# Kernel optimization log

Hardware: AMD Instinct MI355X
Metric: run time of the kernel (lower is better)

The kernel has to match this reference:

```python
import jax, jax.numpy as jnp
import numpy as np

N = 50000
DIM = 512
HID = 256
NCLS = 2
E = 800000


def gcn_conv(x, W, b, src, dst, deg_inv_sqrt, num_nodes):
    # GCNConv (PyG default): h = D^{-1/2} (A + I) D^{-1/2} x W + b
    h = x @ W  # [N, out]
    norm = deg_inv_sqrt[src] * deg_inv_sqrt[dst]  # [E+N]
    msgs = norm[:, None] * h[src]  # gather per edge
    out = jax.ops.segment_sum(msgs, dst, num_segments=num_nodes)
    return out + b


def setup_inputs() -> dict:
    key = jax.random.key(0)
    k1, k2, k3, k4 = jax.random.split(key, 4)
    x = jax.random.normal(k1, (N, DIM), dtype=jnp.float32)
    edge_index = jax.random.randint(k2, (2, E), 0, N, dtype=jnp.int64)
    # Glorot-style init for weights, zero bias (as PyG GCNConv)
    W1 = jax.random.normal(k3, (DIM, HID), dtype=jnp.float32) * (1.0 / np.sqrt(DIM))
    b1 = jnp.zeros((HID,), dtype=jnp.float32)
    W2 = jax.random.normal(k4, (HID, NCLS), dtype=jnp.float32) * (1.0 / np.sqrt(HID))
    b2 = jnp.zeros((NCLS,), dtype=jnp.float32)
    return {"x": x, "W1": W1, "b1": b1, "W2": W2, "b2": b2, "edge_index": edge_index}


def reference(x, W1, b1, W2, b2, edge_index):
    num_nodes = x.shape[0]
    loops = jnp.arange(num_nodes, dtype=edge_index.dtype)
    src = jnp.concatenate([edge_index[0], loops])
    dst = jnp.concatenate([edge_index[1], loops])
    # symmetric normalization with self-loops (edge_weight = 1)
    deg = jax.ops.segment_sum(jnp.ones_like(dst, dtype=x.dtype), dst, num_segments=num_nodes)
    deg_inv_sqrt = jnp.where(deg > 0, jax.lax.rsqrt(deg), 0.0)

    h = gcn_conv(x, W1, b1, src, dst, deg_inv_sqrt, num_nodes)
    h = jax.nn.relu(h)
    # dropout p=0.5 is identity at inference (training=False)
    out = gcn_conv(h, W2, b2, src, dst, deg_inv_sqrt, num_nodes)
    return out
```

## Files before the change

### kernel.cpp

```cpp
#include <hip/hip_runtime.h>
#include <stdint.h>

#define NN   50000
#define DIMK 512
#define HIDN 256
#define NE   800000

#define SCAN_ITEMS 4
#define SCAN_BLK 256
#define SCAN_PER_BLOCK (SCAN_ITEMS * SCAN_BLK)
#define NBLK ((NN + SCAN_PER_BLOCK - 1) / SCAN_PER_BLOCK)

typedef float f32x4  __attribute__((ext_vector_type(4)));
typedef float f32x16 __attribute__((ext_vector_type(16)));
typedef short s16x8  __attribute__((ext_vector_type(8)));

static __device__ __forceinline__ unsigned short f2bf(float f) {
  union { float f; uint32_t u; } v; v.f = f;
  uint32_t u = v.u;
  u += 0x7fffu + ((u >> 16) & 1u);
  return (unsigned short)(u >> 16);
}

static __device__ __forceinline__ uint32_t cvt_pk_bf16(float lo, float hi) {
  uint32_t r;
  asm("v_cvt_pk_bf16_f32 %0, %1, %2" : "=v"(r) : "v"(lo), "v"(hi));
  return r;
}

__global__ void k_hist(const int* __restrict__ edst, int* __restrict__ cnt) {
  int e = blockIdx.x * 256 + threadIdx.x;
  if (e < NE) atomicAdd(&cnt[edst[e]], 1);
}

__global__ __launch_bounds__(256) void k_blocksum(const int* __restrict__ cnt,
                                                  int* __restrict__ blocksum) {
  const int t = threadIdx.x;
  const int base = blockIdx.x * SCAN_PER_BLOCK + t * SCAN_ITEMS;
  int s = 0;
#pragma unroll
  for (int j = 0; j < SCAN_ITEMS; ++j) { int i = base + j; if (i < NN) s += cnt[i]; }
#pragma unroll
  for (int o = 1; o < 64; o <<= 1) s += __shfl_xor(s, o);
  __shared__ int wsum[4];
  if ((t & 63) == 0) wsum[t >> 6] = s;
  __syncthreads();
  if (t == 0) blocksum[blockIdx.x] = wsum[0] + wsum[1] + wsum[2] + wsum[3];
}

__global__ void k_scanblocks(const int* __restrict__ blocksum, int* __restrict__ blockoff) {
  const int t = threadIdx.x;
  int own = (t < NBLK) ? blocksum[t] : 0;
  int v = own;
#pragma unroll
  for (int o = 1; o < 64; o <<= 1) { int u = __shfl_up(v, o); if (t >= o) v += u; }
  if (t < NBLK) blockoff[t] = v - own;
}

__global__ __launch_bounds__(256) void k_finalize(const int* __restrict__ cnt,
                                                  const int* __restrict__ blockoff,
                                                  int* __restrict__ offsets,
                                                  int* __restrict__ cursor,
                                                  float* __restrict__ dis) {
  const int t = threadIdx.x;
  const int l = t & 63, w = t >> 6;
  const int base = blockIdx.x * SCAN_PER_BLOCK + t * SCAN_ITEMS;
  int c[SCAN_ITEMS]; int s = 0;
#pragma unroll
  for (int j = 0; j < SCAN_ITEMS; ++j) { int i = base + j; c[j] = (i < NN) ? cnt[i] : 0; s += c[j]; }
  const int own = s;
#pragma unroll
  for (int o = 1; o < 64; o <<= 1) { int u = __shfl_up(s, o); if (l >= o) s += u; }
  __shared__ int wt[4];
  if (l == 63) wt[w] = s;
  __syncthreads();
  int waveoff = 0;
  for (int ww = 0; ww < w; ++ww) waveoff += wt[ww];
  int run = blockoff[blockIdx.x] + waveoff + (s - own);
#pragma unroll
  for (int j = 0; j < SCAN_ITEMS; ++j) {
    int i = base + j;
    if (i < NN) {
      offsets[i] = run;
      cursor[i]  = run;
      dis[i] = rsqrtf((float)(c[j] + 1));
      run += c[j];
    }
  }
  if (blockIdx.x == 0 && t == 0) offsets[NN] = NE;
}

__global__ void k_scatter(const int* __restrict__ esrc, const int* __restrict__ edst,
                          int* __restrict__ cursor, int* __restrict__ ssorted) {
  int e = blockIdx.x * 256 + threadIdx.x;
  if (e < NE) {
    int d = edst[e];
    int p = atomicAdd(&cursor[d], 1);
    ssorted[p] = esrc[e];
  }
}

__global__ void k_prep_w1t(const float* __restrict__ W1, char* __restrict__ w1t) {
  int tid = blockIdx.x * 256 + threadIdx.x;
  int c  = tid & 255;
  int k  = tid >> 8;
  int t  = k >> 4;
  int kk = k & 15;
  int g  = kk >> 3;
  int i  = kk & 7;
  int j  = c >> 5;
  int cc = c & 31;
  unsigned short v = f2bf(W1[k * HIDN + c]);
  *(unsigned short*)(w1t + (t * 8 + j) * 1024 + (g * 32 + cc) * 16 + i * 2) = v;
}

#define GSTEP(T, AC, BC)                                                        \
  {                                                                             \
    union { s16x8 v; uint32_t u[4]; } AF;                                       \
    AF.u[0] = cvt_pk_bf16(AC[0].x, AC[0].y);                                    \
    AF.u[1] = cvt_pk_bf16(AC[0].z, AC[0].w);                                    \
    AF.u[2] = cvt_pk_bf16(AC[1].x, AC[1].y);                                    \
    AF.u[3] = cvt_pk_bf16(AC[1].z, AC[1].w);                                    \
    _Pragma("unroll")                                                           \
    for (int j = 0; j < 4; ++j)                                                 \
      acc[j] = __builtin_amdgcn_mfma_f32_32x32x16_bf16(AF.v, BC[j], acc[j], 0, 0, 0); \
    if ((T) + 2 < 32) {                                                         \
      _Pragma("unroll")                                                         \
      for (int j = 0; j < 4; ++j)                                               \
        BC[j] = *(const s16x8*)(wb + ((T) + 2) * 8192 + j * 1024);              \
    }                                                                           \
    if ((T) + 4 < 32) {                                                         \
      AC[0] = ap[((T) + 4) * 4];                                                \
      AC[1] = ap[((T) + 4) * 4 + 1];                                            \
    }                                                                           \
  }

__global__ __launch_bounds__(256, 3) void k_gemm1(const float* __restrict__ x,
                                                  const char* __restrict__ w1t,
                                                  const float* __restrict__ dis,
                                                  unsigned short* __restrict__ h1s) {
  const int l = threadIdx.x & 63;
  const int wid = (blockIdx.x * 256 + threadIdx.x) >> 6;
  const int stripe = wid >> 1;
  const int R0 = stripe * 32;
  if (R0 >= NN) return;
  const int j0 = (wid & 1) * 4;
  const int h = l >> 5;
  int ra = R0 + (l & 31);
  if (ra >= NN) ra = NN - 1;

  const float4* ap = (const float4*)(x + (size_t)ra * DIMK) + h * 2;
  const char* wb = w1t + j0 * 1024 + l * 16;

  f32x16 acc[4];
#pragma unroll
  for (int j = 0; j < 4; ++j)
#pragma unroll
    for (int g = 0; g < 16; ++g) acc[j][g] = 0.f;

  float4 A0[2], A1[2], A2[2], A3[2];
  A0[0] = ap[0];  A0[1] = ap[1];
  A1[0] = ap[4];  A1[1] = ap[5];
  A2[0] = ap[8];  A2[1] = ap[9];
  A3[0] = ap[12]; A3[1] = ap[13];
  s16x8 Ba[4], Bb[4];
#pragma unroll
  for (int j = 0; j < 4; ++j) Ba[j] = *(const s16x8*)(wb + j * 1024);
#pragma unroll
  for (int j = 0; j < 4; ++j) Bb[j] = *(const s16x8*)(wb + 8192 + j * 1024);

#pragma unroll
  for (int q = 0; q < 8; ++q) {
    GSTEP(4 * q + 0, A0, Ba);
    GSTEP(4 * q + 1, A1, Bb);
    GSTEP(4 * q + 2, A2, Ba);
    GSTEP(4 * q + 3, A3, Bb);
  }

  const int cc = l & 31;
  float dv[16];
#pragma unroll
  for (int g = 0; g < 16; ++g) {
    int row = R0 + (g & 3) + 8 * (g >> 2) + 4 * h;
    dv[g] = (row < NN) ? dis[row] : 0.f;
  }
#pragma unroll
  for (int j = 0; j < 4; ++j) {
#pragma unroll
    for (int g = 0; g < 16; ++g) {
      int row = R0 + (g & 3) + 8 * (g >> 2) + 4 * h;
      if (row < NN)
        h1s[(size_t)row * HIDN + (j0 + j) * 32 + cc] = f2bf(acc[j][g] * dv[g]);
    }
  }
}

__global__ __launch_bounds__(256) void k_agg1(const unsigned short* __restrict__ h1s,
                                              const int* __restrict__ offsets,
                                              const int* __restrict__ ssorted,
                                              const float* __restrict__ dis,
                                              const float* __restrict__ b1,
                                              const float* __restrict__ W2,
                                              float* __restrict__ h2s) {
  const int w = threadIdx.x >> 6;
  const int l = threadIdx.x & 63;
  const int d = blockIdx.x * 4 + w;
  if (d >= NN) return;

  float a0, a1, a2, a3;
  {
    uint2 v = *(const uint2*)(h1s + (size_t)d * HIDN + l * 4);
    a0 = __uint_as_float(v.x << 16);
    a1 = __uint_as_float(v.x & 0xffff0000u);
    a2 = __uint_as_float(v.y << 16);
    a3 = __uint_as_float(v.y & 0xffff0000u);
  }
  const int off0 = offsets[d], off1 = offsets[d + 1];
  int e = off0;
  for (; e + 4 <= off1; e += 4) {
    int s0 = ssorted[e], s1 = ssorted[e + 1], s2 = ssorted[e + 2], s3 = ssorted[e + 3];
    uint2 v0 = *(const uint2*)(h1s + (size_t)s0 * HIDN + l * 4);
    uint2 v1 = *(const uint2*)(h1s + (size_t)s1 * HIDN + l * 4);
    uint2 v2 = *(const uint2*)(h1s + (size_t)s2 * HIDN + l * 4);
    uint2 v3 = *(const uint2*)(h1s + (size_t)s3 * HIDN + l * 4);
    a0 += __uint_as_float(v0.x << 16) + __uint_as_float(v1.x << 16) +
          __uint_as_float(v2.x << 16) + __uint_as_float(v3.x << 16);
    a1 += __uint_as_float(v0.x & 0xffff0000u) + __uint_as_float(v1.x & 0xffff0000u) +
          __uint_as_float(v2.x & 0xffff0000u) + __uint_as_float(v3.x & 0xffff0000u);
    a2 += __uint_as_float(v0.y << 16) + __uint_as_float(v1.y << 16) +
          __uint_as_float(v2.y << 16) + __uint_as_float(v3.y << 16);
    a3 += __uint_as_float(v0.y & 0xffff0000u) + __uint_as_float(v1.y & 0xffff0000u) +
          __uint_as_float(v2.y & 0xffff0000u) + __uint_as_float(v3.y & 0xffff0000u);
  }
  for (; e < off1; ++e) {
    int s = ssorted[e];
    uint2 v = *(const uint2*)(h1s + (size_t)s * HIDN + l * 4);
    a0 += __uint_as_float(v.x << 16);
    a1 += __uint_as_float(v.x & 0xffff0000u);
    a2 += __uint_as_float(v.y << 16);
    a3 += __uint_as_float(v.y & 0xffff0000u);
  }

  const float dsd = dis[d];
  const int c0 = l * 4;
  float r0 = fmaxf(a0 * dsd + b1[c0 + 0], 0.f);
  float r1 = fmaxf(a1 * dsd + b1[c0 + 1], 0.f);
  float r2 = fmaxf(a2 * dsd + b1[c0 + 2], 0.f);
  float r3 = fmaxf(a3 * dsd + b1[c0 + 3], 0.f);

  float p0 = r0 * W2[(c0 + 0) * 2] + r1 * W2[(c0 + 1) * 2] +
             r2 * W2[(c0 + 2) * 2] + r3 * W2[(c0 + 3) * 2];
  float p1 = r0 * W2[(c0 + 0) * 2 + 1] + r1 * W2[(c0 + 1) * 2 + 1] +
             r2 * W2[(c0 + 2) * 2 + 1] + r3 * W2[(c0 + 3) * 2 + 1];
#pragma unroll
  for (int o = 1; o < 64; o <<= 1) {
    p0 += __shfl_xor(p0, o);
    p1 += __shfl_xor(p1, o);
  }
  if (l == 0) {
    h2s[(size_t)d * 2 + 0] = dsd * p0;
    h2s[(size_t)d * 2 + 1] = dsd * p1;
  }
}

__global__ void k_agg2(const float* __restrict__ h2s, const int* __restrict__ offsets,
                       const int* __restrict__ ssorted, const float* __restrict__ dis,
                       const float* __restrict__ b2, float* __restrict__ out) {
  int d = blockIdx.x * 256 + threadIdx.x;
  if (d >= NN) return;
  float2 sv = *(const float2*)(h2s + (size_t)d * 2);
  float a0 = sv.x, a1 = sv.y;
  int off0 = offsets[d], off1 = offsets[d + 1];
  int e = off0;
  for (; e + 4 <= off1; e += 4) {
    int s0 = ssorted[e], s1 = ssorted[e + 1], s2 = ssorted[e + 2], s3 = ssorted[e + 3];
    float2 v0 = *(const float2*)(h2s + (size_t)s0 * 2);
    float2 v1 = *(const float2*)(h2s + (size_t)s1 * 2);
    float2 v2 = *(const float2*)(h2s + (size_t)s2 * 2);
    float2 v3 = *(const float2*)(h2s + (size_t)s3 * 2);
    a0 += v0.x + v1.x + v2.x + v3.x;
    a1 += v0.y + v1.y + v2.y + v3.y;
  }
  for (; e < off1; ++e) {
    int s = ssorted[e];
    float2 v = *(const float2*)(h2s + (size_t)s * 2);
    a0 += v.x; a1 += v.y;
  }
  float dsd = dis[d];
  out[(size_t)d * 2 + 0] = dsd * a0 + b2[0];
  out[(size_t)d * 2 + 1] = dsd * a1 + b2[1];
}

extern "C" void kernel_launch(void* const* d_in, const int* in_sizes, int n_in,
                              void* d_out, int out_size, void* d_ws, size_t ws_size,
                              hipStream_t stream) {
  (void)in_sizes; (void)n_in; (void)out_size; (void)ws_size;
  const float* x   = (const float*)d_in[0];
  const float* W1  = (const float*)d_in[1];
  const float* b1  = (const float*)d_in[2];
  const float* W2  = (const float*)d_in[3];
  const float* b2  = (const float*)d_in[4];
  const int*   ei  = (const int*)d_in[5];
  const int* esrc = ei;
  const int* edst = ei + NE;
  float* out = (float*)d_out;

  char* ws = (char*)d_ws;
  unsigned short* h1s = (unsigned short*)(ws + 0);
  char*  w1t     = ws + 25600000;
  float* dis     = (float*)(ws + 25862144);
  float* h2s     = (float*)(ws + 26062144);
  int*   cnt     = (int*)(ws + 26462144);
  int*   offsets = (int*)(ws + 26662144);
  int*   cursor  = (int*)(ws + 26862208);
  int*   ssorted = (int*)(ws + 27062208);
  int*   blocksum= (int*)(ws + 30262208);
  int*   blockoff= (int*)(ws + 30262464);

  hipMemsetAsync(cnt, 0, NN * sizeof(int), stream);
  k_hist<<<(NE + 255) / 256, 256, 0, stream>>>(edst, cnt);
  k_blocksum<<<NBLK, 256, 0, stream>>>(cnt, blocksum);
  k_scanblocks<<<1, 64, 0, stream>>>(blocksum, blockoff);
  k_finalize<<<NBLK, 256, 0, stream>>>(cnt, blockoff, offsets, cursor, dis);
  k_scatter<<<(NE + 255) / 256, 256, 0, stream>>>(esrc, edst, cursor, ssorted);
  k_prep_w1t<<<(DIMK * HIDN) / 256, 256, 0, stream>>>(W1, w1t);
  {
    const int nwaves = 2 * ((NN + 31) / 32);
    const int nblk   = (nwaves + 3) / 4;
    k_gemm1<<<nblk, 256, 0, stream>>>(x, w1t, dis, h1s);
  }
  k_agg1<<<(NN + 3) / 4, 256, 0, stream>>>(h1s, offsets, ssorted, dis, b1, W2, h2s);
  k_agg2<<<(NN + 255) / 256, 256, 0, stream>>>(h2s, offsets, ssorted, dis, b2, out);
}
```

Before: 214.8 us.

## Stage x tiles through LDS with coalesced loads in GEMM1, one wave per block

GEMM1 now launches one 64-thread wave per block. It loads x rows cooperatively with coalesced float4 reads into a padded LDS tile (stride 17), prefetching the next K-tile into registers, then reads the MFMA A fragments from LDS. Before, each lane read two float4s directly from its own row, which gave strided uncoalesced accesses. The change adds two barriers per K-tile and LDS traffic, and 64-thread blocks may limit occupancy packing. Both waves of a stripe still load the same x rows independently.

```diff
diff --git a/kernel.cpp b/kernel.cpp
--- a/kernel.cpp
+++ b/kernel.cpp
@@ -114,42 +114,31 @@
   *(unsigned short*)(w1t + (t * 8 + j) * 1024 + (g * 32 + cc) * 16 + i * 2) = v;
 }
 
-#define GSTEP(T, AC, BC)                                                        \
-  {                                                                             \
-    union { s16x8 v; uint32_t u[4]; } AF;                                       \
-    AF.u[0] = cvt_pk_bf16(AC[0].x, AC[0].y);                                    \
-    AF.u[1] = cvt_pk_bf16(AC[0].z, AC[0].w);                                    \
-    AF.u[2] = cvt_pk_bf16(AC[1].x, AC[1].y);                                    \
-    AF.u[3] = cvt_pk_bf16(AC[1].z, AC[1].w);                                    \
-    _Pragma("unroll")                                                           \
-    for (int j = 0; j < 4; ++j)                                                 \
-      acc[j] = __builtin_amdgcn_mfma_f32_32x32x16_bf16(AF.v, BC[j], acc[j], 0, 0, 0); \
-    if ((T) + 2 < 32) {                                                         \
-      _Pragma("unroll")                                                         \
-      for (int j = 0; j < 4; ++j)                                               \
-        BC[j] = *(const s16x8*)(wb + ((T) + 2) * 8192 + j * 1024);              \
-    }                                                                           \
-    if ((T) + 4 < 32) {                                                         \
-      AC[0] = ap[((T) + 4) * 4];                                                \
-      AC[1] = ap[((T) + 4) * 4 + 1];                                            \
-    }                                                                           \
-  }
-
-__global__ __launch_bounds__(256, 3) void k_gemm1(const float* __restrict__ x,
-                                                  const char* __restrict__ w1t,
-                                                  const float* __restrict__ dis,
-                                                  unsigned short* __restrict__ h1s) {
-  const int l = threadIdx.x & 63;
-  const int wid = (blockIdx.x * 256 + threadIdx.x) >> 6;
+__global__ __launch_bounds__(64, 3) void k_gemm1(const float* __restrict__ x,
+                                                 const char* __restrict__ w1t,
+                                                 const float* __restrict__ dis,
+                                                 unsigned short* __restrict__ h1s) {
+  __shared__ float4 lds4[32 * 17];
+  const int l = threadIdx.x;
+  const int wid = blockIdx.x;
   const int stripe = wid >> 1;
   const int R0 = stripe * 32;
-  if (R0 >= NN) return;
   const int j0 = (wid & 1) * 4;
   const int h = l >> 5;
-  int ra = R0 + (l & 31);
-  if (ra >= NN) ra = NN - 1;
-
-  const float4* ap = (const float4*)(x + (size_t)ra * DIMK) + h * 2;
+
+  const int st_r = l >> 4;
+  const int st_s = l & 15;
+  const float4* x4 = (const float4*)x;
+
+  int gidx[8];
+#pragma unroll
+  for (int q = 0; q < 8; ++q) {
+    int row = R0 + q * 4 + st_r;
+    if (row >= NN) row = NN - 1;
+    gidx[q] = row * (DIMK / 4) + st_s;
+  }
+
+  const int r_loc = l & 31;
   const char* wb = w1t + j0 * 1024 + l * 16;
 
   f32x16 acc[4];
@@ -158,23 +147,48 @@
 #pragma unroll
     for (int g = 0; g < 16; ++g) acc[j][g] = 0.f;
 
-  float4 A0[2], A1[2], A2[2], A3[2];
-  A0[0] = ap[0];  A0[1] = ap[1];
-  A1[0] = ap[4];  A1[1] = ap[5];
-  A2[0] = ap[8];  A2[1] = ap[9];
-  A3[0] = ap[12]; A3[1] = ap[13];
-  s16x8 Ba[4], Bb[4];
-#pragma unroll
-  for (int j = 0; j < 4; ++j) Ba[j] = *(const s16x8*)(wb + j * 1024);
-#pragma unroll
-  for (int j = 0; j < 4; ++j) Bb[j] = *(const s16x8*)(wb + 8192 + j * 1024);
-
-#pragma unroll
-  for (int q = 0; q < 8; ++q) {
-    GSTEP(4 * q + 0, A0, Ba);
-    GSTEP(4 * q + 1, A1, Bb);
-    GSTEP(4 * q + 2, A2, Ba);
-    GSTEP(4 * q + 3, A3, Bb);
+  float4 G[8];
+#pragma unroll
+  for (int q = 0; q < 8; ++q) G[q] = x4[gidx[q]];
+
+#pragma unroll
+  for (int kt = 0; kt < 8; ++kt) {
+    __syncthreads();
+#pragma unroll
+    for (int q = 0; q < 8; ++q)
+      lds4[(q * 4 + st_r) * 17 + st_s] = G[q];
+    if (kt < 7) {
+      const int b = (kt + 1) * 16;
+#pragma unroll
+      for (int q = 0; q < 8; ++q) G[q] = x4[gidx[q] + b];
+    }
+    __syncthreads();
+
+    s16x8 Bc[4], Bn[4];
+#pragma unroll
+    for (int j = 0; j < 4; ++j)
+      Bc[j] = *(const s16x8*)(wb + (kt * 4 + 0) * 8192 + j * 1024);
+#pragma unroll
+    for (int ks = 0; ks < 4; ++ks) {
+      if (ks < 3) {
+#pragma unroll
+        for (int j = 0; j < 4; ++j)
+          Bn[j] = *(const s16x8*)(wb + (kt * 4 + ks + 1) * 8192 + j * 1024);
+      }
+      const int slo = ks * 4 + h * 2;
+      const float4 alo = lds4[r_loc * 17 + slo];
+      const float4 ahi = lds4[r_loc * 17 + slo + 1];
+      union { s16x8 v; uint32_t u[4]; } AF;
+      AF.u[0] = cvt_pk_bf16(alo.x, alo.y);
+      AF.u[1] = cvt_pk_bf16(alo.z, alo.w);
+      AF.u[2] = cvt_pk_bf16(ahi.x, ahi.y);
+      AF.u[3] = cvt_pk_bf16(ahi.z, ahi.w);
+#pragma unroll
+      for (int j = 0; j < 4; ++j)
+        acc[j] = __builtin_amdgcn_mfma_f32_32x32x16_bf16(AF.v, Bc[j], acc[j], 0, 0, 0);
+#pragma unroll
+      for (int j = 0; j < 4; ++j) Bc[j] = Bn[j];
+    }
   }
 
   const int cc = l & 31;
@@ -326,8 +340,7 @@
   k_prep_w1t<<<(DIMK * HIDN) / 256, 256, 0, stream>>>(W1, w1t);
   {
     const int nwaves = 2 * ((NN + 31) / 32);
-    const int nblk   = (nwaves + 3) / 4;
-    k_gemm1<<<nblk, 256, 0, stream>>>(x, w1t, dis, h1s);
+    k_gemm1<<<nwaves, 64, 0, stream>>>(x, w1t, dis, h1s);
   }
   k_agg1<<<(NN + 3) / 4, 256, 0, stream>>>(h1s, offsets, ssorted, dis, b1, W2, h2s);
   k_agg2<<<(NN + 255) / 256, 256, 0, stream>>>(h2s, offsets, ssorted, dis, b2, out);
```

Result: slower. 273.1 us (+27.1%).

## Split layer-1 aggregation into column slices with atomic accumulation

Applied to the files above, without the earlier changes.

Layer-1 neighbor aggregation is split into 8 sequential launches, each covering 32 hidden columns, so the gathered feature slice is small enough to stay cache-resident during random gathers. Within a wave, four lane groups process different edges in parallel and are reduced with shuffles. Partial second-layer projections are accumulated into h2s with atomicAdd after a new memset. This trades better gather locality for re-reading the CSR index arrays eight times, extra launches, narrower loads, and nondeterministic float summation order.

```diff
diff --git a/kernel.cpp b/kernel.cpp
--- a/kernel.cpp
+++ b/kernel.cpp
@@ -195,71 +195,55 @@
   }
 }
 
-__global__ __launch_bounds__(256) void k_agg1(const unsigned short* __restrict__ h1s,
-                                              const int* __restrict__ offsets,
-                                              const int* __restrict__ ssorted,
-                                              const float* __restrict__ dis,
-                                              const float* __restrict__ b1,
-                                              const float* __restrict__ W2,
-                                              float* __restrict__ h2s) {
+__global__ __launch_bounds__(256) void k_agg1s(const unsigned short* __restrict__ h1s,
+                                               const int* __restrict__ offsets,
+                                               const int* __restrict__ ssorted,
+                                               const float* __restrict__ dis,
+                                               const float* __restrict__ b1,
+                                               const float* __restrict__ W2,
+                                               float* __restrict__ h2s,
+                                               int slice) {
   const int w = threadIdx.x >> 6;
   const int l = threadIdx.x & 63;
   const int d = blockIdx.x * 4 + w;
   if (d >= NN) return;
-
-  float a0, a1, a2, a3;
+  const int g4 = l >> 4;
+  const int il = l & 15;
+  const uint32_t* base = (const uint32_t*)h1s + slice * 16 + il;
+
+  float a0 = 0.f, a1 = 0.f;
+  const int off0 = offsets[d], off1 = offsets[d + 1];
+  for (int i = off0; i < off1; i += 4) {
+    const int idx = i + g4;
+    if (idx < off1) {
+      const int s = ssorted[idx];
+      const uint32_t v = base[(size_t)s * 128];
+      a0 += __uint_as_float(v << 16);
+      a1 += __uint_as_float(v & 0xffff0000u);
+    }
+  }
+  a0 += __shfl_xor(a0, 16); a0 += __shfl_xor(a0, 32);
+  a1 += __shfl_xor(a1, 16); a1 += __shfl_xor(a1, 32);
   {
-    uint2 v = *(const uint2*)(h1s + (size_t)d * HIDN + l * 4);
-    a0 = __uint_as_float(v.x << 16);
-    a1 = __uint_as_float(v.x & 0xffff0000u);
-    a2 = __uint_as_float(v.y << 16);
-    a3 = __uint_as_float(v.y & 0xffff0000u);
-  }
-  const int off0 = offsets[d], off1 = offsets[d + 1];
-  int e = off0;
-  for (; e + 4 <= off1; e += 4) {
-    int s0 = ssorted[e], s1 = ssorted[e + 1], s2 = ssorted[e + 2], s3 = ssorted[e + 3];
-    uint2 v0 = *(const uint2*)(h1s + (size_t)s0 * HIDN + l * 4);
-    uint2 v1 = *(const uint2*)(h1s + (size_t)s1 * HIDN + l * 4);
-    uint2 v2 = *(const uint2*)(h1s + (size_t)s2 * HIDN + l * 4);
-    uint2 v3 = *(const uint2*)(h1s + (size_t)s3 * HIDN + l * 4);
-    a0 += __uint_as_float(v0.x << 16) + __uint_as_float(v1.x << 16) +
-          __uint_as_float(v2.x << 16) + __uint_as_float(v3.x << 16);
-    a1 += __uint_as_float(v0.x & 0xffff0000u) + __uint_as_float(v1.x & 0xffff0000u) +
-          __uint_as_float(v2.x & 0xffff0000u) + __uint_as_float(v3.x & 0xffff0000u);
-    a2 += __uint_as_float(v0.y << 16) + __uint_as_float(v1.y << 16) +
-          __uint_as_float(v2.y << 16) + __uint_as_float(v3.y << 16);
-    a3 += __uint_as_float(v0.y & 0xffff0000u) + __uint_as_float(v1.y & 0xffff0000u) +
-          __uint_as_float(v2.y & 0xffff0000u) + __uint_as_float(v3.y & 0xffff0000u);
-  }
-  for (; e < off1; ++e) {
-    int s = ssorted[e];
-    uint2 v = *(const uint2*)(h1s + (size_t)s * HIDN + l * 4);
-    a0 += __uint_as_float(v.x << 16);
-    a1 += __uint_as_float(v.x & 0xffff0000u);
-    a2 += __uint_as_float(v.y << 16);
-    a3 += __uint_as_float(v.y & 0xffff0000u);
+    const uint32_t v = base[(size_t)d * 128];
+    a0 += __uint_as_float(v << 16);
+    a1 += __uint_as_float(v & 0xffff0000u);
   }
 
   const float dsd = dis[d];
-  const int c0 = l * 4;
-  float r0 = fmaxf(a0 * dsd + b1[c0 + 0], 0.f);
-  float r1 = fmaxf(a1 * dsd + b1[c0 + 1], 0.f);
-  float r2 = fmaxf(a2 * dsd + b1[c0 + 2], 0.f);
-  float r3 = fmaxf(a3 * dsd + b1[c0 + 3], 0.f);
-
-  float p0 = r0 * W2[(c0 + 0) * 2] + r1 * W2[(c0 + 1) * 2] +
-             r2 * W2[(c0 + 2) * 2] + r3 * W2[(c0 + 3) * 2];
-  float p1 = r0 * W2[(c0 + 0) * 2 + 1] + r1 * W2[(c0 + 1) * 2 + 1] +
-             r2 * W2[(c0 + 2) * 2 + 1] + r3 * W2[(c0 + 3) * 2 + 1];
-#pragma unroll
-  for (int o = 1; o < 64; o <<= 1) {
+  const int c0 = slice * 32 + il * 2;
+  const float r0 = fmaxf(a0 * dsd + b1[c0 + 0], 0.f);
+  const float r1 = fmaxf(a1 * dsd + b1[c0 + 1], 0.f);
+  float p0 = r0 * W2[(c0 + 0) * 2] + r1 * W2[(c0 + 1) * 2];
+  float p1 = r0 * W2[(c0 + 0) * 2 + 1] + r1 * W2[(c0 + 1) * 2 + 1];
+#pragma unroll
+  for (int o = 1; o < 16; o <<= 1) {
     p0 += __shfl_xor(p0, o);
     p1 += __shfl_xor(p1, o);
   }
   if (l == 0) {
-    h2s[(size_t)d * 2 + 0] = dsd * p0;
-    h2s[(size_t)d * 2 + 1] = dsd * p1;
+    atomicAdd(&h2s[(size_t)d * 2 + 0], dsd * p0);
+    atomicAdd(&h2s[(size_t)d * 2 + 1], dsd * p1);
   }
 }
 
@@ -318,6 +302,7 @@
   int*   blockoff= (int*)(ws + 30262464);
 
   hipMemsetAsync(cnt, 0, NN * sizeof(int), stream);
+  hipMemsetAsync(h2s, 0, NN * 2 * sizeof(float), stream);
   k_hist<<<(NE + 255) / 256, 256, 0, stream>>>(edst, cnt);
   k_blocksum<<<NBLK, 256, 0, stream>>>(cnt, blocksum);
   k_scanblocks<<<1, 64, 0, stream>>>(blocksum, blockoff);
@@ -329,6 +314,7 @@
     const int nblk   = (nwaves + 3) / 4;
     k_gemm1<<<nblk, 256, 0, stream>>>(x, w1t, dis, h1s);
   }
-  k_agg1<<<(NN + 3) / 4, 256, 0, stream>>>(h1s, offsets, ssorted, dis, b1, W2, h2s);
+  for (int s = 0; s < 8; ++s)
+    k_agg1s<<<(NN + 3) / 4, 256, 0, stream>>>(h1s, offsets, ssorted, dis, b1, W2, h2s, s);
   k_agg2<<<(NN + 255) / 256, 256, 0, stream>>>(h2s, offsets, ssorted, dis, b2, out);
 }
```

Result: slower. 413.5 us (+92.5%).
